# Kernel optimization log

Measured on AMD Instinct MI355X. Metric: run time of the kernel, lower is better.

## Reference

```python
import jax, jax.numpy as jnp
import numpy as np
from functools import partial

EPS = 1e-5
SCALE = 2
NUM_BLOCKS = 2


def _layernorm(x, g, b):
    mu = jnp.mean(x, axis=-1, keepdims=True)
    var = jnp.var(x, axis=-1, keepdims=True)
    return (x - mu) * jax.lax.rsqrt(var + EPS) * g + b


def _rwkv(tokens, td, Wk, Wv, Wr, Wo, ln_g, ln_b):
    # tokens: (B, N, C)
    x = _layernorm(tokens, ln_g, ln_b)
    k = jnp.einsum('bnc,oc->bno', x, Wk)
    v = jnp.einsum('bnc,oc->bno', x, Wv)
    r = jax.nn.sigmoid(jnp.einsum('bnc,oc->bno', x, Wr))
    decay = jnp.exp(-jax.nn.relu(td))  # (C,)

    def step(state, inp):
        kt, vt, rt = inp  # each (B, C)
        state = state * decay + kt
        return state, rt * (state + vt)

    B, N, C = tokens.shape
    init = jnp.zeros((B, C), dtype=tokens.dtype)
    # scan over token axis
    _, yT = jax.lax.scan(step, init, (k.transpose(1, 0, 2), v.transpose(1, 0, 2), r.transpose(1, 0, 2)))
    y = yT.transpose(1, 0, 2)  # (B, N, C)
    return jnp.einsum('bnc,oc->bno', y, Wo)


def reference(x, global_state, cond_gw, cond_gb, cond_bw, cond_bb,
              td, Wk, Wv, Wr, Wo, ln_g, ln_b, gp_w, gp_b, bp_w, bp_b):
    B, C, H, W = x.shape
    Hp, Wp = H * SCALE, W * SCALE
    # bilinear upsample, half-pixel centers == torch align_corners=False
    x_up = jax.image.resize(x, (B, C, Hp, Wp), method='bilinear')
    tokens = x_up.reshape(B, C, Hp * Wp).transpose(0, 2, 1)  # (B, N, C)
    # semantic conditioning (FiLM from global state)
    gamma = (global_state @ cond_gw.T + cond_gb)[:, None, :]
    beta = (global_state @ cond_bw.T + cond_bb)[:, None, :]
    tokens = tokens * (1.0 + gamma) + beta

    out = x_up
    cur = tokens
    for i in range(NUM_BLOCKS):
        if i > 0:
            cur = out.reshape(B, C, Hp * Wp).transpose(0, 2, 1)
        t = _rwkv(cur, td[i], Wk[i], Wv[i], Wr[i], Wo[i], ln_g[i], ln_b[i])
        g = jnp.einsum('bnc,oc->bno', t, gp_w[i]) + gp_b[i]
        bt = jnp.einsum('bnc,oc->bno', t, bp_w[i]) + bp_b[i]
        g = g.transpose(0, 2, 1).reshape(B, C, Hp, Wp)
        bt = bt.transpose(0, 2, 1).reshape(B, C, Hp, Wp)
        out = out * (1.0 + jnp.tanh(g)) + bt
    return out


def setup_inputs() -> dict:
    key = jax.random.key(0)
    ks = jax.random.split(key, 16)
    B, C, H, W = 8, 128, 64, 64
    w_scale = 0.02
    inp = {
        'x': jax.random.normal(ks[0], (B, C, H, W), jnp.float32),
        'global_state': jax.random.normal(ks[1], (B, C), jnp.float32),
        'cond_gw': jax.random.normal(ks[2], (C, C), jnp.float32) * w_scale,
        'cond_gb': jnp.zeros((C,), jnp.float32),
        'cond_bw': jax.random.normal(ks[3], (C, C), jnp.float32) * w_scale,
        'cond_bb': jnp.zeros((C,), jnp.float32),
        'td': jax.random.uniform(ks[4], (NUM_BLOCKS, C), jnp.float32),
        'Wk': jax.random.normal(ks[5], (NUM_BLOCKS, C, C), jnp.float32) * w_scale,
        'Wv': jax.random.normal(ks[6], (NUM_BLOCKS, C, C), jnp.float32) * w_scale,
        'Wr': jax.random.normal(ks[7], (NUM_BLOCKS, C, C), jnp.float32) * w_scale,
        'Wo': jax.random.normal(ks[8], (NUM_BLOCKS, C, C), jnp.float32) * w_scale,
        'ln_g': jnp.ones((NUM_BLOCKS, C), jnp.float32),
        'ln_b': jnp.zeros((NUM_BLOCKS, C), jnp.float32),
        'gp_w': jax.random.normal(ks[9], (NUM_BLOCKS, C, C), jnp.float32) * w_scale,
        'gp_b': jnp.zeros((NUM_BLOCKS, C), jnp.float32),
        'bp_w': jax.random.normal(ks[10], (NUM_BLOCKS, C, C), jnp.float32) * w_scale,
        'bp_b': jnp.zeros((NUM_BLOCKS, C), jnp.float32),
    }
    return inp
```

## Files before the change

### kernel.cpp

```cpp
#include <hip/hip_runtime.h>
#include <hip/hip_bf16.h>

#define BB 8
#define CC 128
#define NN 16384
#define MM (BB * NN)
#define NCH 128
#define CLN 128

typedef __attribute__((ext_vector_type(8))) short short8;
typedef __attribute__((ext_vector_type(4))) float floatx4;
typedef unsigned short u16;
typedef unsigned int u32;

__device__ __forceinline__ float bf2f(u16 h) {
  u32 u = ((u32)h) << 16;
  return __builtin_bit_cast(float, u);
}
__device__ __forceinline__ u16 f2bf(float f) {
  u32 u = __builtin_bit_cast(u32, f);
  u32 r = u + 0x7FFFu + ((u >> 16) & 1u);
  return (u16)(r >> 16);
}

__global__ void film_kernel(const float* __restrict__ gs, const float* __restrict__ gw,
                            const float* __restrict__ gb, const float* __restrict__ bw,
                            const float* __restrict__ bb, float* __restrict__ gamma,
                            float* __restrict__ beta) {
  int idx = blockIdx.x * 256 + threadIdx.x;
  int b = idx >> 7, c = idx & 127;
  float sg = 0.f, sb = 0.f;
  for (int j = 0; j < 128; ++j) {
    float g = gs[b * 128 + j];
    sg += g * gw[c * 128 + j];
    sb += g * bw[c * 128 + j];
  }
  gamma[idx] = sg + gb[c];
  beta[idx] = sb + bb[c];
}

__global__ void convert_kernel(const float* __restrict__ Wk, const float* __restrict__ Wv,
                               const float* __restrict__ Wr, const float* __restrict__ Wo,
                               const float* __restrict__ gp, const float* __restrict__ bp,
                               u16* __restrict__ dst) {
  int idx = blockIdx.x * 256 + threadIdx.x;
  int which = idx >> 15;
  int off = idx & 32767;
  const float* s;
  switch (which) {
    case 0: s = Wk; break; case 1: s = Wv; break; case 2: s = Wr; break;
    case 3: s = Wo; break; case 4: s = gp; break; default: s = bp; break;
  }
  dst[idx] = f2bf(s[off]);
}

template <int UPS>
__global__ __launch_bounds__(256) void prep_kernel(
    const float* __restrict__ src, const float* __restrict__ gamma,
    const float* __restrict__ beta, const float* __restrict__ lng,
    const float* __restrict__ lnb, float* __restrict__ outp, u16* __restrict__ xn) {
  __shared__ float tile[64][129];
  __shared__ float smu[64], srs[64];
  int bidx = blockIdx.x;
  int half = bidx & 1;
  int ho = (bidx >> 1) & 127;
  int b = bidx >> 8;
  int wo0 = half * 64;
  int tid = threadIdx.x;
  int tk = tid & 63;
  int wo = wo0 + tk;
  int c0 = tid >> 6;
  int j0 = 0, j1 = 0, i0 = 0, i1 = 0;
  float wy0 = 0.f, wy1 = 0.f, wx0 = 0.f, wx1 = 0.f;
  if (UPS) {
    int jj = ho >> 1;
    if ((ho & 1) == 0) { j0 = jj > 0 ? jj - 1 : 0; j1 = jj; wy0 = 0.25f; wy1 = 0.75f; }
    else               { j0 = jj; j1 = jj < 63 ? jj + 1 : 63; wy0 = 0.75f; wy1 = 0.25f; }
    int ii = wo >> 1;
    if ((wo & 1) == 0) { i0 = ii > 0 ? ii - 1 : 0; i1 = ii; wx0 = 0.25f; wx1 = 0.75f; }
    else               { i0 = ii; i1 = ii < 63 ? ii + 1 : 63; wx0 = 0.75f; wx1 = 0.25f; }
  }
  for (int it = 0; it < 32; ++it) {
    int c = it * 4 + c0;
    float v;
    if (UPS) {
      const float* xp = src + ((size_t)(b * 128 + c)) * 4096;
      v = wy0 * (wx0 * xp[j0 * 64 + i0] + wx1 * xp[j0 * 64 + i1]) +
          wy1 * (wx0 * xp[j1 * 64 + i0] + wx1 * xp[j1 * 64 + i1]);
      outp[((size_t)(b * 128 + c)) * 16384 + ho * 128 + wo] = v;
      v = v * (1.f + gamma[b * 128 + c]) + beta[b * 128 + c];
    } else {
      v = src[((size_t)(b * 128 + c)) * 16384 + ho * 128 + wo];
    }
    tile[tk][c] = v;
  }
  __syncthreads();
  {
    int token = tid >> 2, q = tid & 3;
    float s = 0.f, s2 = 0.f;
    for (int j = 0; j < 32; ++j) { float v = tile[token][q * 32 + j]; s += v; s2 += v * v; }
    s += __shfl_xor(s, 1); s2 += __shfl_xor(s2, 1);
    s += __shfl_xor(s, 2); s2 += __shfl_xor(s2, 2);
    if (q == 0) {
      float mu = s * 0.0078125f;
      float var = s2 * 0.0078125f - mu * mu;
      smu[token] = mu;
      srs[token] = rsqrtf(var + 1e-5f);
    }
  }
  __syncthreads();
  size_t base = ((size_t)b * 16384 + ho * 128 + wo0) * 128;
  for (int it = 0; it < 32; ++it) {
    int idx = it * 256 + tid;
    int token = idx >> 7, c = idx & 127;
    float v = (tile[token][c] - smu[token]) * srs[token] * lng[c] + lnb[c];
    xn[base + idx] = f2bf(v);
  }
}

__global__ __launch_bounds__(256) void gemm_S_kernel(
    const u16* __restrict__ A, const u16* __restrict__ W0,
    const float* __restrict__ td, float* __restrict__ Sbuf) {
  __shared__ u16 Alds[128 * 128];
  __shared__ u16 Wlds[128 * 128];
  __shared__ float Sred[512];
  int tid = threadIdx.x;
  int wave = tid >> 6, lane = tid & 63;
  int l15 = lane & 15, l4 = lane >> 4;
  size_t row0 = (size_t)blockIdx.x * 128;
#pragma unroll
  for (int it = 0; it < 8; ++it) {
    int idx = it * 256 + tid;
    int rr = idx >> 4, s = idx & 15;
    uint4 d = *(const uint4*)(A + (row0 + rr) * 128 + s * 8);
    *(uint4*)(&Alds[rr * 128 + ((s ^ (rr & 15)) << 3)]) = d;
  }
#pragma unroll
  for (int it = 0; it < 8; ++it) {
    int idx = it * 256 + tid;
    int rr = idx >> 4, s = idx & 15;
    uint4 d = *(const uint4*)(W0 + rr * 128 + s * 8);
    *(uint4*)(&Wlds[rr * 128 + ((s ^ (rr & 15)) << 3)]) = d;
  }
  __syncthreads();
  floatx4 acc[2][8];
#pragma unroll
  for (int mi = 0; mi < 2; ++mi)
#pragma unroll
    for (int ni = 0; ni < 8; ++ni) acc[mi][ni] = (floatx4){0.f, 0.f, 0.f, 0.f};
#pragma unroll
  for (int kk = 0; kk < 4; ++kk) {
    int seg = kk * 4 + l4;
    short8 a0 = *(const short8*)(&Alds[(wave * 32 + l15) * 128 + ((seg ^ l15) << 3)]);
    short8 a1 = *(const short8*)(&Alds[(wave * 32 + 16 + l15) * 128 + ((seg ^ l15) << 3)]);
#pragma unroll
    for (int ni = 0; ni < 8; ++ni) {
      short8 bfr = *(const short8*)(&Wlds[(ni * 16 + l15) * 128 + ((seg ^ l15) << 3)]);
      acc[0][ni] = __builtin_amdgcn_mfma_f32_16x16x32_bf16(a0, bfr, acc[0][ni], 0, 0, 0);
      acc[1][ni] = __builtin_amdgcn_mfma_f32_16x16x32_bf16(a1, bfr, acc[1][ni], 0, 0, 0);
    }
  }
  int T0 = wave * 32 + l4 * 4;
#pragma unroll
  for (int ni = 0; ni < 8; ++ni) {
    int c = ni * 16 + l15;
    float a = fmaxf(td[c], 0.f);
    float E = __expf(-a * (float)(127 - T0));
    float r1 = __expf(a);
    float r16 = __expf(a * 16.f);
    float w = E, sum;
    sum  = w * acc[0][ni][0]; w *= r1;
    sum += w * acc[0][ni][1]; w *= r1;
    sum += w * acc[0][ni][2]; w *= r1;
    sum += w * acc[0][ni][3];
    w = E * r16;
    sum += w * acc[1][ni][0]; w *= r1;
    sum += w * acc[1][ni][1]; w *= r1;
    sum += w * acc[1][ni][2]; w *= r1;
    sum += w * acc[1][ni][3];
    sum += __shfl_xor(sum, 16);
    sum += __shfl_xor(sum, 32);
    if (l4 == 0) Sred[wave * 128 + c] = sum;
  }
  __syncthreads();
  if (tid < 128) {
    float s = Sred[tid] + Sred[128 + tid] + Sred[256 + tid] + Sred[384 + tid];
    Sbuf[(blockIdx.x & 127) * 1024 + (blockIdx.x >> 7) * 128 + tid] = s;
  }
}

__global__ __launch_bounds__(256) void scan2_kernel(const float* __restrict__ S,
                                                    const float* __restrict__ td,
                                                    float* __restrict__ init) {
  int wave = threadIdx.x >> 6, lane = threadIdx.x & 63;
  int bc = blockIdx.x * 4 + wave;
  int c = bc & 127;
  float a1 = __expf(-fmaxf(td[c], 0.f) * 128.f);
  float s0 = S[(2 * lane) * 1024 + bc];
  float s1 = S[(2 * lane + 1) * 1024 + bc];
  float s = s1 + a1 * s0;
  float a = a1 * a1;
  for (int off = 1; off < 64; off <<= 1) {
    float ss = __shfl_up(s, off);
    float aa = __shfl_up(a, off);
    if (lane >= off) { s = s + a * ss; a = a * aa; }
  }
  float e = __shfl_up(s, 1);
  if (lane == 0) e = 0.f;
  init[(2 * lane) * 1024 + bc] = e;
  init[(2 * lane + 1) * 1024 + bc] = a1 * e + s0;
}

__global__ __launch_bounds__(256, 2) void gemm_y_kernel(
    const u16* __restrict__ A, const u16* __restrict__ Wv_, const u16* __restrict__ Wr_,
    const u16* __restrict__ Wk_, const float* __restrict__ td,
    const float* __restrict__ init_, u16* __restrict__ outY) {
  __shared__ u16 Alds[128 * 128];
  __shared__ u16 Wlds[128 * 128];
  __shared__ float SWT[512];
  __shared__ float ILS[128];
  int tid = threadIdx.x;
  int wave = tid >> 6, lane = tid & 63;
  int l15 = lane & 15, l4 = lane >> 4;
  size_t row0 = (size_t)blockIdx.x * 128;
  int bI = blockIdx.x >> 7, chunkI = blockIdx.x & 127;
  if (tid < 128) ILS[tid] = init_[chunkI * 1024 + bI * 128 + tid];

#pragma unroll
  for (int it = 0; it < 8; ++it) {
    int idx = it * 256 + tid;
    int rr = idx >> 4, s = idx & 15;
    uint4 d = *(const uint4*)(A + (row0 + rr) * 128 + s * 8);
    *(uint4*)(&Alds[rr * 128 + ((s ^ (rr & 15)) << 3)]) = d;
  }
#pragma unroll
  for (int it = 0; it < 8; ++it) {
    int idx = it * 256 + tid;
    int rr = idx >> 4, s = idx & 15;
    uint4 d = *(const uint4*)(Wv_ + rr * 128 + s * 8);
    *(uint4*)(&Wlds[rr * 128 + ((s ^ (rr & 15)) << 3)]) = d;
  }
  float dd[8], d4a[8];
#pragma unroll
  for (int ni = 0; ni < 8; ++ni) {
    float a = fmaxf(td[ni * 16 + l15], 0.f);
    float d = __expf(-a);
    dd[ni] = d;
    float d2 = d * d;
    d4a[ni] = d2 * d2;
  }
  __syncthreads();

  floatx4 accv[2][8];
#pragma unroll
  for (int mi = 0; mi < 2; ++mi)
#pragma unroll
    for (int ni = 0; ni < 8; ++ni) accv[mi][ni] = (floatx4){0.f, 0.f, 0.f, 0.f};
#pragma unroll
  for (int kk = 0; kk < 4; ++kk) {
    int seg = kk * 4 + l4;
    short8 a0 = *(const short8*)(&Alds[(wave * 32 + l15) * 128 + ((seg ^ l15) << 3)]);
    short8 a1 = *(const short8*)(&Alds[(wave * 32 + 16 + l15) * 128 + ((seg ^ l15) << 3)]);
#pragma unroll
    for (int ni = 0; ni < 8; ++ni) {
      short8 bfr = *(const short8*)(&Wlds[(ni * 16 + l15) * 128 + ((seg ^ l15) << 3)]);
      accv[0][ni] = __builtin_amdgcn_mfma_f32_16x16x32_bf16(a0, bfr, accv[0][ni], 0, 0, 0);
      accv[1][ni] = __builtin_amdgcn_mfma_f32_16x16x32_bf16(a1, bfr, accv[1][ni], 0, 0, 0);
    }
  }
  __syncthreads();
#pragma unroll
  for (int it = 0; it < 8; ++it) {
    int idx = it * 256 + tid;
    int rr = idx >> 4, s = idx & 15;
    uint4 d = *(const uint4*)(Wr_ + rr * 128 + s * 8);
    *(uint4*)(&Wlds[rr * 128 + ((s ^ (rr & 15)) << 3)]) = d;
  }
  __syncthreads();
  floatx4 accr[2][8];
#pragma unroll
  for (int mi = 0; mi < 2; ++mi)
#pragma unroll
    for (int ni = 0; ni < 8; ++ni) accr[mi][ni] = (floatx4){0.f, 0.f, 0.f, 0.f};
#pragma unroll
  for (int kk = 0; kk < 4; ++kk) {
    int seg = kk * 4 + l4;
    short8 a0 = *(const short8*)(&Alds[(wave * 32 + l15) * 128 + ((seg ^ l15) << 3)]);
    short8 a1 = *(const short8*)(&Alds[(wave * 32 + 16 + l15) * 128 + ((seg ^ l15) << 3)]);
#pragma unroll
    for (int ni = 0; ni < 8; ++ni) {
      short8 bfr = *(const short8*)(&Wlds[(ni * 16 + l15) * 128 + ((seg ^ l15) << 3)]);
      accr[0][ni] = __builtin_amdgcn_mfma_f32_16x16x32_bf16(a0, bfr, accr[0][ni], 0, 0, 0);
      accr[1][ni] = __builtin_amdgcn_mfma_f32_16x16x32_bf16(a1, bfr, accr[1][ni], 0, 0, 0);
    }
  }
  u32 rvp[2][8][2], rp[2][8][2];
#pragma unroll
  for (int mi = 0; mi < 2; ++mi) {
#pragma unroll
    for (int ni = 0; ni < 8; ++ni) {
      float rs[4], rv[4];
#pragma unroll
      for (int j = 0; j < 4; ++j) {
        float sg = 1.f / (1.f + __expf(-accr[mi][ni][j]));
        rs[j] = sg;
        rv[j] = sg * accv[mi][ni][j];
      }
      rvp[mi][ni][0] = (u32)f2bf(rv[0]) | ((u32)f2bf(rv[1]) << 16);
      rvp[mi][ni][1] = (u32)f2bf(rv[2]) | ((u32)f2bf(rv[3]) << 16);
      rp[mi][ni][0] = (u32)f2bf(rs[0]) | ((u32)f2bf(rs[1]) << 16);
      rp[mi][ni][1] = (u32)f2bf(rs[2]) | ((u32)f2bf(rs[3]) << 16);
    }
  }
  __syncthreads();
#pragma unroll
  for (int it = 0; it < 8; ++it) {
    int idx = it * 256 + tid;
    int rr = idx >> 4, s = idx & 15;
    uint4 d = *(const uint4*)(Wk_ + rr * 128 + s * 8);
    *(uint4*)(&Wlds[rr * 128 + ((s ^ (rr & 15)) << 3)]) = d;
  }
  __syncthreads();
  floatx4 acck[2][8];
#pragma unroll
  for (int mi = 0; mi < 2; ++mi)
#pragma unroll
    for (int ni = 0; ni < 8; ++ni) acck[mi][ni] = (floatx4){0.f, 0.f, 0.f, 0.f};
#pragma unroll
  for (int kk = 0; kk < 4; ++kk) {
    int seg = kk * 4 + l4;
    short8 a0 = *(const short8*)(&Alds[(wave * 32 + l15) * 128 + ((seg ^ l15) << 3)]);
    short8 a1 = *(const short8*)(&Alds[(wave * 32 + 16 + l15) * 128 + ((seg ^ l15) << 3)]);
#pragma unroll
    for (int ni = 0; ni < 8; ++ni) {
      short8 bfr = *(const short8*)(&Wlds[(ni * 16 + l15) * 128 + ((seg ^ l15) << 3)]);
      acck[0][ni] = __builtin_amdgcn_mfma_f32_16x16x32_bf16(a0, bfr, acck[0][ni], 0, 0, 0);
      acck[1][ni] = __builtin_amdgcn_mfma_f32_16x16x32_bf16(a1, bfr, acck[1][ni], 0, 0, 0);
    }
  }
  float Elr[2][8];
  float B0r[8];
#pragma unroll
  for (int ni = 0; ni < 8; ++ni) {
    float d = dd[ni], d4 = d4a[ni];
    float d8 = d4 * d4, d16 = d8 * d8;
    float I[2];
#pragma unroll
    for (int mi = 0; mi < 2; ++mi) {
      float p0 = acck[mi][ni][0];
      float p1 = d * p0 + acck[mi][ni][1];
      float p2 = d * p1 + acck[mi][ni][2];
      float p3 = d * p2 + acck[mi][ni][3];
      acck[mi][ni][0] = p0; acck[mi][ni][1] = p1;
      acck[mi][ni][2] = p2; acck[mi][ni][3] = p3;
      float Iv = p3;
      float t1 = __shfl_up(Iv, 16);
      if (l4 >= 1) Iv += d4 * t1;
      float t2 = __shfl_up(Iv, 32);
      if (l4 >= 2) Iv += d8 * t2;
      float ex = __shfl_up(Iv, 16);
      Elr[mi][ni] = (l4 == 0) ? 0.f : ex;
      I[mi] = Iv;
    }
    float B0 = __shfl(I[0], 48 + l15);
    float B1 = __shfl(I[1], 48 + l15);
    B0r[ni] = B0;
    if (l4 == 0) SWT[wave * 128 + ni * 16 + l15] = B1 + d16 * B0;
  }
  __syncthreads();
  u16* YW = Wlds;
#pragma unroll
  for (int ni = 0; ni < 8; ++ni) {
    int c = ni * 16 + l15;
    float d = dd[ni], d4 = d4a[ni];
    float d8 = d4 * d4, d12 = d8 * d4, d16 = d8 * d8, d32 = d16 * d16;
    float e = ILS[c];
#pragma unroll
    for (int wv = 0; wv < 3; ++wv)
      if (wv < wave) e = e * d32 + SWT[wv * 128 + c];
    float d4l = (l4 == 0) ? 1.f : ((l4 == 1) ? d4 : ((l4 == 2) ? d8 : d12));
#pragma unroll
    for (int mi = 0; mi < 2; ++mi) {
      float Emi = (mi == 0) ? e : (e * d16 + B0r[ni]);
      float Sb = Elr[mi][ni] + d4l * Emi;
      float w = d;
#pragma unroll
      for (int j = 0; j < 4; ++j) {
        float s = acck[mi][ni][j] + w * Sb;
        w *= d;
        float rvv = bf2f((u16)(rvp[mi][ni][j >> 1] >> ((j & 1) * 16)));
        float rss = bf2f((u16)(rp[mi][ni][j >> 1] >> ((j & 1) * 16)));
        float y = rvv + rss * s;
        int row = wave * 32 + mi * 16 + l4 * 4 + j;
        int colsw = c ^ (((row >> 2) & 3) << 4);
        YW[row * 128 + colsw] = f2bf(y);
      }
    }
  }
  __syncthreads();
#pragma unroll
  for (int it = 0; it < 8; ++it) {
    int idx = it * 256 + tid;
    int row = idx >> 4, cb = (idx & 15) * 8;
    int csw = cb ^ (((row >> 2) & 3) << 4);
    uint4 dv = *(const uint4*)(&YW[row * 128 + csw]);
    *(uint4*)(outY + (row0 + row) * 128 + cb) = dv;
  }
}

__global__ __launch_bounds__(512, 4) void tail_kernel(
    const u16* __restrict__ yl,
    const u16* __restrict__ Wo, const u16* __restrict__ Wg, const u16* __restrict__ Wb,
    const float* __restrict__ gpb, const float* __restrict__ bpb,
    float* __restrict__ outp) {
  __shared__ u32 SMEM[8192];
  u16* Y = (u16*)SMEM;
  u16* T2 = (u16*)SMEM;
  u32* MB = SMEM;

  int tid = threadIdx.x;
  int wave = tid >> 6, lane = tid & 63;
  int l15 = lane & 15, l4 = lane >> 4;
  int b = blockIdx.x >> 7;
  int chunk = blockIdx.x & 127;
  size_t ebase = ((size_t)b * 16384 + (size_t)chunk * 128) * 128;

#pragma unroll
  for (int it = 0; it < 4; ++it) {
    int idx = it * 512 + tid;
    int t = idx >> 4;
    int c8 = (idx & 15) * 8;
    uint4 yv = *(const uint4*)(yl + ebase + (size_t)t * 128 + c8);
    *(uint4*)(&Y[t * 128 + (((c8 >> 3) ^ (t & 15)) << 3)]) = yv;
  }
  __syncthreads();

  int ob = wave * 16;
  short8 wof[4];
#pragma unroll
  for (int kk = 0; kk < 4; ++kk)
    wof[kk] = *(const short8*)(Wo + (ob + l15) * 128 + kk * 32 + l4 * 8);
  floatx4 acc[8];
#pragma unroll
  for (int ni = 0; ni < 8; ++ni) acc[ni] = (floatx4){0.f, 0.f, 0.f, 0.f};
#pragma unroll
  for (int kk = 0; kk < 4; ++kk) {
    int seg = kk * 4 + l4;
#pragma unroll
    for (int ni = 0; ni < 8; ++ni) {
      short8 yf = *(const short8*)(&Y[(ni * 16 + l15) * 128 + ((seg ^ l15) << 3)]);
      acc[ni] = __builtin_amdgcn_mfma_f32_16x16x32_bf16(wof[kk], yf, acc[ni], 0, 0, 0);
    }
  }
  __syncthreads();

#pragma unroll
  for (int ni = 0; ni < 8; ++ni) {
    int tok = ni * 16 + l15;
#pragma unroll
    for (int j = 0; j < 4; j += 2) {
      int o = ob + l4 * 4 + j;
      u32 pack = (u32)f2bf(acc[ni][j]) | ((u32)f2bf(acc[ni][j + 1]) << 16);
      int pos = tok * 128 + ((((o >> 3) ^ (tok & 15)) << 3) | (o & 7));
      *(u32*)(T2 + pos) = pack;
    }
  }
  __syncthreads();

  short8 wgf[4], wbf2[4];
#pragma unroll
  for (int kk = 0; kk < 4; ++kk) {
    wgf[kk]  = *(const short8*)(Wg + (ob + l15) * 128 + kk * 32 + l4 * 8);
    wbf2[kk] = *(const short8*)(Wb + (ob + l15) * 128 + kk * 32 + l4 * 8);
  }
  floatx4 ag[8], ab[8];
#pragma unroll
  for (int ni = 0; ni < 8; ++ni) {
    ag[ni] = (floatx4){0.f, 0.f, 0.f, 0.f};
    ab[ni] = (floatx4){0.f, 0.f, 0.f, 0.f};
  }
#pragma unroll
  for (int kk = 0; kk < 4; ++kk) {
    int seg = kk * 4 + l4;
#pragma unroll
    for (int ni = 0; ni < 8; ++ni) {
      short8 tf = *(const short8*)(&T2[(ni * 16 + l15) * 128 + ((seg ^ l15) << 3)]);
      ag[ni] = __builtin_amdgcn_mfma_f32_16x16x32_bf16(wgf[kk], tf, ag[ni], 0, 0, 0);
      ab[ni] = __builtin_amdgcn_mfma_f32_16x16x32_bf16(wbf2[kk], tf, ab[ni], 0, 0, 0);
    }
  }
  __syncthreads();

#pragma unroll
  for (int h = 0; h < 2; ++h) {
    if ((wave >> 2) == h) {
      int orel0 = (wave & 3) * 16;
#pragma unroll
      for (int ni = 0; ni < 8; ++ni) {
        int tok = ni * 16 + l15;
#pragma unroll
        for (int j = 0; j < 4; ++j) {
          int orel = orel0 + l4 * 4 + j;
          int o = h * 64 + orel;
          float g = ag[ni][j] + gpb[o];
          float t1 = __expf(2.f * g);
          float m = 2.f - 2.f / (t1 + 1.f);
          float bt = ab[ni][j] + bpb[o];
          int rot = ((orel & 3) << 2) | ((orel >> 2) & 3);
          MB[orel * 128 + ((((tok >> 3) ^ rot) << 3) | (tok & 7))] =
              (u32)f2bf(m) | ((u32)f2bf(bt) << 16);
        }
      }
    }
    __syncthreads();
#pragma unroll
    for (int it = 0; it < 2; ++it) {
      int idx = it * 512 + tid;
      int orel = idx >> 4, seg = idx & 15;
      int o = h * 64 + orel;
      int rot = ((orel & 3) << 2) | ((orel >> 2) & 3);
      int sp = ((seg ^ rot) << 3);
      uint4 mb0 = *(const uint4*)(&MB[orel * 128 + sp]);
      uint4 mb1 = *(const uint4*)(&MB[orel * 128 + sp + 4]);
      float* op = outp + ((size_t)(b * 128 + o)) * 16384 + chunk * 128 + seg * 8;
      float4 o0 = *(float4*)op;
      float4 o1 = *(float4*)(op + 4);
      o0.x = o0.x * bf2f((u16)(mb0.x & 0xffff)) + bf2f((u16)(mb0.x >> 16));
      o0.y = o0.y * bf2f((u16)(mb0.y & 0xffff)) + bf2f((u16)(mb0.y >> 16));
      o0.z = o0.z * bf2f((u16)(mb0.z & 0xffff)) + bf2f((u16)(mb0.z >> 16));
      o0.w = o0.w * bf2f((u16)(mb0.w & 0xffff)) + bf2f((u16)(mb0.w >> 16));
      o1.x = o1.x * bf2f((u16)(mb1.x & 0xffff)) + bf2f((u16)(mb1.x >> 16));
      o1.y = o1.y * bf2f((u16)(mb1.y & 0xffff)) + bf2f((u16)(mb1.y >> 16));
      o1.z = o1.z * bf2f((u16)(mb1.z & 0xffff)) + bf2f((u16)(mb1.z >> 16));
      o1.w = o1.w * bf2f((u16)(mb1.w & 0xffff)) + bf2f((u16)(mb1.w >> 16));
      *(float4*)op = o0;
      *(float4*)(op + 4) = o1;
    }
    __syncthreads();
  }
}

extern "C" void kernel_launch(void* const* d_in, const int* in_sizes, int n_in,
                              void* d_out, int out_size, void* d_ws, size_t ws_size,
                              hipStream_t stream) {
  const float* x        = (const float*)d_in[0];
  const float* gs       = (const float*)d_in[1];
  const float* cond_gw  = (const float*)d_in[2];
  const float* cond_gb  = (const float*)d_in[3];
  const float* cond_bw  = (const float*)d_in[4];
  const float* cond_bb  = (const float*)d_in[5];
  const float* td       = (const float*)d_in[6];
  const float* Wk       = (const float*)d_in[7];
  const float* Wv       = (const float*)d_in[8];
  const float* Wr       = (const float*)d_in[9];
  const float* Wo       = (const float*)d_in[10];
  const float* ln_g     = (const float*)d_in[11];
  const float* ln_b     = (const float*)d_in[12];
  const float* gp_w     = (const float*)d_in[13];
  const float* gp_b     = (const float*)d_in[14];
  const float* bp_w     = (const float*)d_in[15];
  const float* bp_b     = (const float*)d_in[16];
  float* outp = (float*)d_out;

  char* w = (char*)d_ws;
  float* gamma = (float*)w; w += 4096;
  float* beta  = (float*)w; w += 4096;
  u16* wbf     = (u16*)w;   w += 6 * 2 * 16384 * sizeof(u16);
  u16* xn      = (u16*)w;   w += (size_t)MM * 128 * sizeof(u16);
  u16* ybuf    = (u16*)w;   w += (size_t)MM * 128 * sizeof(u16);
  float* Sbuf  = (float*)w; w += NCH * 1024 * sizeof(float);
  float* ibuf  = (float*)w; w += NCH * 1024 * sizeof(float);

  film_kernel<<<4, 256, 0, stream>>>(gs, cond_gw, cond_gb, cond_bw, cond_bb, gamma, beta);
  convert_kernel<<<768, 256, 0, stream>>>(Wk, Wv, Wr, Wo, gp_w, bp_w, wbf);

  for (int blk = 0; blk < 2; ++blk) {
    const u16* bWk = wbf + 0 * 32768 + blk * 16384;
    const u16* bWv = wbf + 1 * 32768 + blk * 16384;
    const u16* bWr = wbf + 2 * 32768 + blk * 16384;
    const u16* bWo = wbf + 3 * 32768 + blk * 16384;
    const u16* bGp = wbf + 4 * 32768 + blk * 16384;
    const u16* bBp = wbf + 5 * 32768 + blk * 16384;
    const float* tdi = td + blk * 128;

    if (blk == 0)
      prep_kernel<1><<<2048, 256, 0, stream>>>(x, gamma, beta, ln_g, ln_b, outp, xn);
    else
      prep_kernel<0><<<2048, 256, 0, stream>>>(outp, nullptr, nullptr, ln_g + 128,
                                               ln_b + 128, nullptr, xn);

    gemm_S_kernel<<<1024, 256, 0, stream>>>(xn, bWk, tdi, Sbuf);
    scan2_kernel<<<256, 256, 0, stream>>>(Sbuf, tdi, ibuf);
    gemm_y_kernel<<<1024, 256, 0, stream>>>(xn, bWv, bWr, bWk, tdi, ibuf, ybuf);
    tail_kernel<<<1024, 512, 0, stream>>>(ybuf, bWo, bGp, bBp,
                                          gp_b + blk * 128, bp_b + blk * 128, outp);
  }
}
```

Before: 277.1 us.

## Fuse gemm_y and tail kernels so y stays in LDS

Merges the y-producing GEMM/scan kernel with the output-projection/gate tail kernel, so y is written swizzled into shared memory and consumed directly instead of round-tripping through a global bf16 buffer. The tail's GEMMs are re-tiled for 4 waves (each wave handles 32 output channels), and the gate and bias GEMMs run sequentially to bound register pressure. This drops one launch and about 32 MB of global traffic per block, at the cost of a 256-thread kernel with higher register use and launch_bounds relaxed to a single argument, which may lower occupancy.

```diff
diff --git a/kernel.cpp b/kernel.cpp
--- a/kernel.cpp
+++ b/kernel.cpp
@@ -211,20 +211,27 @@
   init[(2 * lane + 1) * 1024 + bc] = a1 * e + s0;
 }
 
-__global__ __launch_bounds__(256, 2) void gemm_y_kernel(
+__global__ __launch_bounds__(256) void fused_kernel(
     const u16* __restrict__ A, const u16* __restrict__ Wv_, const u16* __restrict__ Wr_,
     const u16* __restrict__ Wk_, const float* __restrict__ td,
-    const float* __restrict__ init_, u16* __restrict__ outY) {
+    const float* __restrict__ init_,
+    const u16* __restrict__ Wo, const u16* __restrict__ Wg, const u16* __restrict__ Wb,
+    const float* __restrict__ gpb, const float* __restrict__ bpb,
+    float* __restrict__ outp) {
   __shared__ u16 Alds[128 * 128];
   __shared__ u16 Wlds[128 * 128];
   __shared__ float SWT[512];
   __shared__ float ILS[128];
+  u16* T2 = Alds;
+  u16* Y = Wlds;
+  u32* MB = (u32*)Wlds;
+
   int tid = threadIdx.x;
   int wave = tid >> 6, lane = tid & 63;
   int l15 = lane & 15, l4 = lane >> 4;
   size_t row0 = (size_t)blockIdx.x * 128;
-  int bI = blockIdx.x >> 7, chunkI = blockIdx.x & 127;
-  if (tid < 128) ILS[tid] = init_[chunkI * 1024 + bI * 128 + tid];
+  int b = blockIdx.x >> 7, chunk = blockIdx.x & 127;
+  if (tid < 128) ILS[tid] = init_[chunk * 1024 + b * 128 + tid];
 
 #pragma unroll
   for (int it = 0; it < 8; ++it) {
@@ -246,8 +253,7 @@
     float a = fmaxf(td[ni * 16 + l15], 0.f);
     float d = __expf(-a);
     dd[ni] = d;
-    float d2 = d * d;
-    d4a[ni] = d2 * d2;
+    d4a[ni] = d * d * d * d;
   }
   __syncthreads();
 
@@ -368,10 +374,10 @@
     if (l4 == 0) SWT[wave * 128 + ni * 16 + l15] = B1 + d16 * B0;
   }
   __syncthreads();
-  u16* YW = Wlds;
 #pragma unroll
   for (int ni = 0; ni < 8; ++ni) {
     int c = ni * 16 + l15;
+    int chi = c >> 3, clo = c & 7;
     float d = dd[ni], d4 = d4a[ni];
     float d8 = d4 * d4, d12 = d8 * d4, d16 = d8 * d8, d32 = d16 * d16;
     float e = ILS[c];
@@ -392,130 +398,140 @@
         float rss = bf2f((u16)(rp[mi][ni][j >> 1] >> ((j & 1) * 16)));
         float y = rvv + rss * s;
         int row = wave * 32 + mi * 16 + l4 * 4 + j;
-        int colsw = c ^ (((row >> 2) & 3) << 4);
-        YW[row * 128 + colsw] = f2bf(y);
+        Y[row * 128 + (((chi ^ (row & 15)) << 3) | clo)] = f2bf(y);
       }
     }
   }
   __syncthreads();
-#pragma unroll
-  for (int it = 0; it < 8; ++it) {
-    int idx = it * 256 + tid;
-    int row = idx >> 4, cb = (idx & 15) * 8;
-    int csw = cb ^ (((row >> 2) & 3) << 4);
-    uint4 dv = *(const uint4*)(&YW[row * 128 + csw]);
-    *(uint4*)(outY + (row0 + row) * 128 + cb) = dv;
-  }
-}
-
-__global__ __launch_bounds__(512, 4) void tail_kernel(
-    const u16* __restrict__ yl,
-    const u16* __restrict__ Wo, const u16* __restrict__ Wg, const u16* __restrict__ Wb,
-    const float* __restrict__ gpb, const float* __restrict__ bpb,
-    float* __restrict__ outp) {
-  __shared__ u32 SMEM[8192];
-  u16* Y = (u16*)SMEM;
-  u16* T2 = (u16*)SMEM;
-  u32* MB = SMEM;
-
-  int tid = threadIdx.x;
-  int wave = tid >> 6, lane = tid & 63;
-  int l15 = lane & 15, l4 = lane >> 4;
-  int b = blockIdx.x >> 7;
-  int chunk = blockIdx.x & 127;
-  size_t ebase = ((size_t)b * 16384 + (size_t)chunk * 128) * 128;
-
-#pragma unroll
-  for (int it = 0; it < 4; ++it) {
-    int idx = it * 512 + tid;
-    int t = idx >> 4;
-    int c8 = (idx & 15) * 8;
-    uint4 yv = *(const uint4*)(yl + ebase + (size_t)t * 128 + c8);
-    *(uint4*)(&Y[t * 128 + (((c8 >> 3) ^ (t & 15)) << 3)]) = yv;
-  }
-  __syncthreads();
-
-  int ob = wave * 16;
-  short8 wof[4];
-#pragma unroll
-  for (int kk = 0; kk < 4; ++kk)
-    wof[kk] = *(const short8*)(Wo + (ob + l15) * 128 + kk * 32 + l4 * 8);
-  floatx4 acc[8];
-#pragma unroll
-  for (int ni = 0; ni < 8; ++ni) acc[ni] = (floatx4){0.f, 0.f, 0.f, 0.f};
-#pragma unroll
-  for (int kk = 0; kk < 4; ++kk) {
-    int seg = kk * 4 + l4;
-#pragma unroll
-    for (int ni = 0; ni < 8; ++ni) {
-      short8 yf = *(const short8*)(&Y[(ni * 16 + l15) * 128 + ((seg ^ l15) << 3)]);
-      acc[ni] = __builtin_amdgcn_mfma_f32_16x16x32_bf16(wof[kk], yf, acc[ni], 0, 0, 0);
-    }
-  }
-  __syncthreads();
-
-#pragma unroll
-  for (int ni = 0; ni < 8; ++ni) {
-    int tok = ni * 16 + l15;
-#pragma unroll
-    for (int j = 0; j < 4; j += 2) {
-      int o = ob + l4 * 4 + j;
-      u32 pack = (u32)f2bf(acc[ni][j]) | ((u32)f2bf(acc[ni][j + 1]) << 16);
-      int pos = tok * 128 + ((((o >> 3) ^ (tok & 15)) << 3) | (o & 7));
-      *(u32*)(T2 + pos) = pack;
-    }
-  }
-  __syncthreads();
-
-  short8 wgf[4], wbf2[4];
-#pragma unroll
-  for (int kk = 0; kk < 4; ++kk) {
-    wgf[kk]  = *(const short8*)(Wg + (ob + l15) * 128 + kk * 32 + l4 * 8);
-    wbf2[kk] = *(const short8*)(Wb + (ob + l15) * 128 + kk * 32 + l4 * 8);
-  }
-  floatx4 ag[8], ab[8];
-#pragma unroll
-  for (int ni = 0; ni < 8; ++ni) {
-    ag[ni] = (floatx4){0.f, 0.f, 0.f, 0.f};
-    ab[ni] = (floatx4){0.f, 0.f, 0.f, 0.f};
-  }
-#pragma unroll
-  for (int kk = 0; kk < 4; ++kk) {
-    int seg = kk * 4 + l4;
-#pragma unroll
-    for (int ni = 0; ni < 8; ++ni) {
-      short8 tf = *(const short8*)(&T2[(ni * 16 + l15) * 128 + ((seg ^ l15) << 3)]);
-      ag[ni] = __builtin_amdgcn_mfma_f32_16x16x32_bf16(wgf[kk], tf, ag[ni], 0, 0, 0);
-      ab[ni] = __builtin_amdgcn_mfma_f32_16x16x32_bf16(wbf2[kk], tf, ab[ni], 0, 0, 0);
-    }
-  }
-  __syncthreads();
-
-#pragma unroll
-  for (int h = 0; h < 2; ++h) {
-    if ((wave >> 2) == h) {
-      int orel0 = (wave & 3) * 16;
+
+  int ob = wave * 32;
+  {
+    short8 wof[2][4];
+#pragma unroll
+    for (int mi = 0; mi < 2; ++mi)
+#pragma unroll
+      for (int kk = 0; kk < 4; ++kk)
+        wof[mi][kk] = *(const short8*)(Wo + (ob + mi * 16 + l15) * 128 + kk * 32 + l4 * 8);
+    floatx4 a1[2][8];
+#pragma unroll
+    for (int mi = 0; mi < 2; ++mi)
+#pragma unroll
+      for (int ni = 0; ni < 8; ++ni) a1[mi][ni] = (floatx4){0.f, 0.f, 0.f, 0.f};
+#pragma unroll
+    for (int kk = 0; kk < 4; ++kk) {
+      int seg = kk * 4 + l4;
+#pragma unroll
+      for (int ni = 0; ni < 8; ++ni) {
+        short8 yf = *(const short8*)(&Y[(ni * 16 + l15) * 128 + ((seg ^ l15) << 3)]);
+        a1[0][ni] = __builtin_amdgcn_mfma_f32_16x16x32_bf16(wof[0][kk], yf, a1[0][ni], 0, 0, 0);
+        a1[1][ni] = __builtin_amdgcn_mfma_f32_16x16x32_bf16(wof[1][kk], yf, a1[1][ni], 0, 0, 0);
+      }
+    }
+#pragma unroll
+    for (int mi = 0; mi < 2; ++mi)
 #pragma unroll
       for (int ni = 0; ni < 8; ++ni) {
         int tok = ni * 16 + l15;
 #pragma unroll
-        for (int j = 0; j < 4; ++j) {
-          int orel = orel0 + l4 * 4 + j;
-          int o = h * 64 + orel;
-          float g = ag[ni][j] + gpb[o];
-          float t1 = __expf(2.f * g);
-          float m = 2.f - 2.f / (t1 + 1.f);
-          float bt = ab[ni][j] + bpb[o];
-          int rot = ((orel & 3) << 2) | ((orel >> 2) & 3);
-          MB[orel * 128 + ((((tok >> 3) ^ rot) << 3) | (tok & 7))] =
-              (u32)f2bf(m) | ((u32)f2bf(bt) << 16);
+        for (int j = 0; j < 4; j += 2) {
+          int o = ob + mi * 16 + l4 * 4 + j;
+          u32 pack = (u32)f2bf(a1[mi][ni][j]) | ((u32)f2bf(a1[mi][ni][j + 1]) << 16);
+          int pos = tok * 128 + ((((o >> 3) ^ (tok & 15)) << 3) | (o & 7));
+          *(u32*)(T2 + pos) = pack;
         }
       }
+  }
+  __syncthreads();
+
+  u32 pm[2][8][2];
+  {
+    short8 wgf[2][4];
+#pragma unroll
+    for (int mi = 0; mi < 2; ++mi)
+#pragma unroll
+      for (int kk = 0; kk < 4; ++kk)
+        wgf[mi][kk] = *(const short8*)(Wg + (ob + mi * 16 + l15) * 128 + kk * 32 + l4 * 8);
+    floatx4 ag[2][8];
+#pragma unroll
+    for (int mi = 0; mi < 2; ++mi)
+#pragma unroll
+      for (int ni = 0; ni < 8; ++ni) ag[mi][ni] = (floatx4){0.f, 0.f, 0.f, 0.f};
+#pragma unroll
+    for (int kk = 0; kk < 4; ++kk) {
+      int seg = kk * 4 + l4;
+#pragma unroll
+      for (int ni = 0; ni < 8; ++ni) {
+        short8 tf = *(const short8*)(&T2[(ni * 16 + l15) * 128 + ((seg ^ l15) << 3)]);
+        ag[0][ni] = __builtin_amdgcn_mfma_f32_16x16x32_bf16(wgf[0][kk], tf, ag[0][ni], 0, 0, 0);
+        ag[1][ni] = __builtin_amdgcn_mfma_f32_16x16x32_bf16(wgf[1][kk], tf, ag[1][ni], 0, 0, 0);
+      }
+    }
+#pragma unroll
+    for (int mi = 0; mi < 2; ++mi)
+#pragma unroll
+      for (int ni = 0; ni < 8; ++ni) {
+        float mm[4];
+#pragma unroll
+        for (int j = 0; j < 4; ++j) {
+          int o = ob + mi * 16 + l4 * 4 + j;
+          float g = ag[mi][ni][j] + gpb[o];
+          float t1 = __expf(2.f * g);
+          mm[j] = 2.f - 2.f / (t1 + 1.f);
+        }
+        pm[mi][ni][0] = (u32)f2bf(mm[0]) | ((u32)f2bf(mm[1]) << 16);
+        pm[mi][ni][1] = (u32)f2bf(mm[2]) | ((u32)f2bf(mm[3]) << 16);
+      }
+  }
+
+  floatx4 ab[2][8];
+  {
+    short8 wbf2[2][4];
+#pragma unroll
+    for (int mi = 0; mi < 2; ++mi)
+#pragma unroll
+      for (int kk = 0; kk < 4; ++kk)
+        wbf2[mi][kk] = *(const short8*)(Wb + (ob + mi * 16 + l15) * 128 + kk * 32 + l4 * 8);
+#pragma unroll
+    for (int mi = 0; mi < 2; ++mi)
+#pragma unroll
+      for (int ni = 0; ni < 8; ++ni) ab[mi][ni] = (floatx4){0.f, 0.f, 0.f, 0.f};
+#pragma unroll
+    for (int kk = 0; kk < 4; ++kk) {
+      int seg = kk * 4 + l4;
+#pragma unroll
+      for (int ni = 0; ni < 8; ++ni) {
+        short8 tf = *(const short8*)(&T2[(ni * 16 + l15) * 128 + ((seg ^ l15) << 3)]);
+        ab[0][ni] = __builtin_amdgcn_mfma_f32_16x16x32_bf16(wbf2[0][kk], tf, ab[0][ni], 0, 0, 0);
+        ab[1][ni] = __builtin_amdgcn_mfma_f32_16x16x32_bf16(wbf2[1][kk], tf, ab[1][ni], 0, 0, 0);
+      }
+    }
+  }
+  __syncthreads();
+
+#pragma unroll
+  for (int h = 0; h < 2; ++h) {
+    if ((wave >> 1) == h) {
+#pragma unroll
+      for (int mi = 0; mi < 2; ++mi)
+#pragma unroll
+        for (int ni = 0; ni < 8; ++ni) {
+          int tok = ni * 16 + l15;
+#pragma unroll
+          for (int j = 0; j < 4; ++j) {
+            int orel = (wave & 1) * 32 + mi * 16 + l4 * 4 + j;
+            int o = h * 64 + orel;
+            u16 m16 = (u16)(pm[mi][ni][j >> 1] >> ((j & 1) * 16));
+            float bt = ab[mi][ni][j] + bpb[o];
+            int rot = ((orel & 3) << 2) | ((orel >> 2) & 3);
+            MB[orel * 128 + ((((tok >> 3) ^ rot) << 3) | (tok & 7))] =
+                (u32)m16 | ((u32)f2bf(bt) << 16);
+          }
+        }
     }
     __syncthreads();
 #pragma unroll
-    for (int it = 0; it < 2; ++it) {
-      int idx = it * 512 + tid;
+    for (int it = 0; it < 4; ++it) {
+      int idx = it * 256 + tid;
       int orel = idx >> 4, seg = idx & 15;
       int o = h * 64 + orel;
       int rot = ((orel & 3) << 2) | ((orel >> 2) & 3);
@@ -567,7 +583,6 @@
   float* beta  = (float*)w; w += 4096;
   u16* wbf     = (u16*)w;   w += 6 * 2 * 16384 * sizeof(u16);
   u16* xn      = (u16*)w;   w += (size_t)MM * 128 * sizeof(u16);
-  u16* ybuf    = (u16*)w;   w += (size_t)MM * 128 * sizeof(u16);
   float* Sbuf  = (float*)w; w += NCH * 1024 * sizeof(float);
   float* ibuf  = (float*)w; w += NCH * 1024 * sizeof(float);
 
@@ -591,8 +606,8 @@
 
     gemm_S_kernel<<<1024, 256, 0, stream>>>(xn, bWk, tdi, Sbuf);
     scan2_kernel<<<256, 256, 0, stream>>>(Sbuf, tdi, ibuf);
-    gemm_y_kernel<<<1024, 256, 0, stream>>>(xn, bWv, bWr, bWk, tdi, ibuf, ybuf);
-    tail_kernel<<<1024, 512, 0, stream>>>(ybuf, bWo, bGp, bBp,
-                                          gp_b + blk * 128, bp_b + blk * 128, outp);
-  }
-}
+    fused_kernel<<<1024, 256, 0, stream>>>(xn, bWv, bWr, bWk, tdi, ibuf,
+                                           bWo, bGp, bBp, gp_b + blk * 128,
+                                           bp_b + blk * 128, outp);
+  }
+}
```

After: 302.8 us. 1.09x slower.
